# Kernel optimization log

Measured on AMD Instinct MI355X. Metric: run time of the kernel, lower is better.

The kernel has to match this reference:

```python
import jax, jax.numpy as jnp
import numpy as np

N, E = 100000, 800000
H, C = 4, 32
HC = H * C


def setup_inputs() -> dict:
    key = jax.random.key(0)
    ks = jax.random.split(key, 32)

    def lin(k, fi, fo):
        return jax.random.normal(k, (fi, fo), jnp.float32) / np.sqrt(fi)

    inp = {
        "x": jax.random.normal(ks[0], (N, 2), jnp.float32),
        "edge_index": jax.random.randint(ks[1], (2, E), 0, N, jnp.int64),
        "edge_attr": jax.random.normal(ks[2], (E, 1), jnp.float32),
        # layer 0 (in=2)
        "Wq0": lin(ks[3], 2, HC), "bq0": jnp.zeros((HC,), jnp.float32),
        "Wk0": lin(ks[4], 2, HC), "bk0": jnp.zeros((HC,), jnp.float32),
        "Wv0": lin(ks[5], 2, HC), "bv0": jnp.zeros((HC,), jnp.float32),
        "We0": lin(ks[6], 1, HC),
        "Ws0": lin(ks[7], 2, HC), "bs0": jnp.zeros((HC,), jnp.float32),
        # layer 1 (in=HC)
        "Wq1": lin(ks[8], HC, HC), "bq1": jnp.zeros((HC,), jnp.float32),
        "Wk1": lin(ks[9], HC, HC), "bk1": jnp.zeros((HC,), jnp.float32),
        "Wv1": lin(ks[10], HC, HC), "bv1": jnp.zeros((HC,), jnp.float32),
        "We1": lin(ks[11], 1, HC),
        "Ws1": lin(ks[12], HC, HC), "bs1": jnp.zeros((HC,), jnp.float32),
        # classifier
        "Wc1": lin(ks[13], HC, 128), "bc1": jnp.zeros((128,), jnp.float32),
        "Wc2": lin(ks[14], 128, 64), "bc2": jnp.zeros((64,), jnp.float32),
        "Wc3": lin(ks[15], 64, 1), "bc3": jnp.zeros((1,), jnp.float32),
    }
    return inp


def _tconv(x, src, dst, edge_attr, Wq, bq, Wk, bk, Wv, bv, We, Ws, bs):
    # PyG TransformerConv (concat=True, root_weight=True, beta=False)
    n = x.shape[0]
    q = (x @ Wq + bq).reshape(n, H, C)
    k = (x @ Wk + bk).reshape(n, H, C)
    v = (x @ Wv + bv).reshape(n, H, C)
    e = (edge_attr @ We).reshape(-1, H, C)            # [E,H,C]
    k_j = k[src] + e
    v_j = v[src] + e
    alpha = jnp.einsum("ehc,ehc->eh", q[dst], k_j) / np.sqrt(C)  # [E,H]
    m = jax.ops.segment_max(alpha, dst, num_segments=n)          # [n,H]
    m = jnp.where(jnp.isfinite(m), m, 0.0)            # nodes with no in-edges
    ex = jnp.exp(alpha - m[dst])
    denom = jax.ops.segment_sum(ex, dst, num_segments=n)
    w = ex / (denom[dst] + 1e-16)                      # per-edge softmax weight
    out = jax.ops.segment_sum(v_j * w[:, :, None], dst, num_segments=n)
    return out.reshape(n, HC) + x @ Ws + bs


def reference(x, edge_index, edge_attr,
              Wq0, bq0, Wk0, bk0, Wv0, bv0, We0, Ws0, bs0,
              Wq1, bq1, Wk1, bk1, Wv1, bv1, We1, Ws1, bs1,
              Wc1, bc1, Wc2, bc2, Wc3, bc3):
    src, dst = edge_index[0], edge_index[1]
    h = jax.nn.relu(_tconv(x, src, dst, edge_attr, Wq0, bq0, Wk0, bk0, Wv0, bv0, We0, Ws0, bs0))
    h = jax.nn.relu(_tconv(h, src, dst, edge_attr, Wq1, bq1, Wk1, bk1, Wv1, bv1, We1, Ws1, bs1))
    # classifier (dropout inactive in eval)
    h = jax.nn.relu(h @ Wc1 + bc1)
    h = jax.nn.relu(h @ Wc2 + bc2)
    return h @ Wc3 + bc3
```

## Files before the change

kernel.cpp:

```cpp
#include <hip/hip_runtime.h>
#include <hip/hip_bf16.h>
#include <cstdio>
#include <cstdint>


typedef short s16x8 __attribute__((ext_vector_type(8)));
typedef float f32x4 __attribute__((ext_vector_type(4)));

static inline int cdiv(int a, int b) { return (a + b - 1) / b; }

#define EXP2F(x) __builtin_amdgcn_exp2f(x)
#define LOG2E 1.4426950408889634f
#define RSC 0.17677669529663687f

__device__ __forceinline__ float bflo(unsigned u) {
    union { unsigned i; float f; } x; x.i = u << 16; return x.f;
}
__device__ __forceinline__ float bfhi(unsigned u) {
    union { unsigned i; float f; } x; x.i = u & 0xffff0000u; return x.f;
}
__device__ __forceinline__ unsigned short f2b(float f) {
    __hip_bfloat16 h = __float2bfloat16(f);
    return *reinterpret_cast<unsigned short*>(&h);
}
__device__ __forceinline__ unsigned packbf(float lo, float hi) {
    return (unsigned)f2b(lo) | ((unsigned)f2b(hi) << 16);
}


__global__ __launch_bounds__(256) void hist_kernel(const int* __restrict__ dst, int E,
                                                   int* __restrict__ counts) {
    int e = blockIdx.x * 256 + threadIdx.x;
    if (e < E) atomicAdd(&counts[dst[e]], 1);
}

__global__ __launch_bounds__(256) void scan_sums(const int* __restrict__ counts, int n,
                                                 int* __restrict__ bsums) {
    __shared__ int red[256];
    int base = blockIdx.x * 2048 + threadIdx.x * 8;
    int s = 0;
#pragma unroll
    for (int j = 0; j < 8; ++j) {
        int i = base + j;
        if (i < n) s += counts[i];
    }
    red[threadIdx.x] = s;
    __syncthreads();
    for (int off = 128; off > 0; off >>= 1) {
        if (threadIdx.x < off) red[threadIdx.x] += red[threadIdx.x + off];
        __syncthreads();
    }
    if (threadIdx.x == 0) bsums[blockIdx.x] = red[0];
}

__global__ void scan_mid(int* bsums, int nb, int* offsets, int n) {
    if (blockIdx.x == 0 && threadIdx.x == 0) {
        int run = 0;
        for (int i = 0; i < nb; ++i) { int t = bsums[i]; bsums[i] = run; run += t; }
        offsets[n] = run;
    }
}

__global__ __launch_bounds__(256) void scan_out(const int* __restrict__ counts, int n,
                                                const int* __restrict__ bsums,
                                                int* __restrict__ offsets) {
    __shared__ int tsum[256];
    int base = blockIdx.x * 2048 + threadIdx.x * 8;
    int v[8];
    int s = 0;
#pragma unroll
    for (int j = 0; j < 8; ++j) {
        int i = base + j;
        v[j] = (i < n) ? counts[i] : 0;
        s += v[j];
    }
    tsum[threadIdx.x] = s;
    __syncthreads();
    for (int off = 1; off < 256; off <<= 1) {
        int x = (threadIdx.x >= (unsigned)off) ? tsum[threadIdx.x - off] : 0;
        __syncthreads();
        tsum[threadIdx.x] += x;
        __syncthreads();
    }
    int excl = tsum[threadIdx.x] - s + bsums[blockIdx.x];
#pragma unroll
    for (int j = 0; j < 8; ++j) {
        int i = base + j;
        if (i < n) { offsets[i] = excl; excl += v[j]; }
    }
}

__global__ __launch_bounds__(256) void scatter_kernel(const int* __restrict__ src,
                                                      const int* __restrict__ dst,
                                                      const float* __restrict__ ea, int E,
                                                      const int* __restrict__ offsets,
                                                      int* __restrict__ counts,
                                                      int* __restrict__ csr_off,
                                                      float* __restrict__ csr_ea) {
    int e = blockIdx.x * 256 + threadIdx.x;
    if (e >= E) return;
    int d = dst[e];
    int r = atomicSub(&counts[d], 1);
    int p = offsets[d] + r - 1;
    csr_off[p] = src[e] << 9;
    csr_ea[p] = ea[e];
}


__global__ __launch_bounds__(256) void pack_w_kernel(
    const float* __restrict__ Wq1, const float* __restrict__ Wk1,
    const float* __restrict__ Wv1, const float* __restrict__ Ws1,
    const float* __restrict__ Wc1, const float* __restrict__ Wc2,
    unsigned short* __restrict__ wpk,
    const float* __restrict__ Wq0, const float* __restrict__ bq0,
    const float* __restrict__ Wk0, const float* __restrict__ bk0,
    const float* __restrict__ We0, float* __restrict__ gcoef) {
    if (blockIdx.x == 352) {
        int t = threadIdx.x;
        if (t < 48) {
            int h = t / 12, r = t % 12, i = r >> 2, j = r & 3;
            const float* A = (i == 0) ? Wq0 : (i == 1) ? (Wq0 + 128) : bq0;
            const float* B = (j == 0) ? Wk0 : (j == 1) ? (Wk0 + 128) : (j == 2) ? We0 : bk0;
            float s = 0.f;
            for (int c = 0; c < 32; ++c) s += A[h * 32 + c] * B[h * 32 + c];
            gcoef[h * 12 + i * 4 + j] = s * (RSC * LOG2E);
        }
        return;
    }
    int idx = blockIdx.x * 256 + threadIdx.x;
    int local, COLS;
    const float* W;
    if (idx < 81920) {
        int m = idx >> 14;
        local = idx & 16383;
        COLS = 128;
        W = (m == 0) ? Wq1 : (m == 1) ? Wk1 : (m == 2) ? Wv1 : (m == 3) ? Ws1 : Wc1;
    } else {
        local = idx - 81920;
        COLS = 64;
        W = Wc2;
    }
    int CT = COLS >> 4;
    int j = local & 7, lane = (local >> 3) & 63, t = local >> 9;
    int ct = t % CT, kc = t / CT;
    int k = kc * 32 + ((lane >> 4) << 3) + j;
    int nn = (ct << 4) + (lane & 15);
    wpk[idx] = f2b(W[k * COLS + nn]);
}


__global__ __launch_bounds__(256) void agg0_kernel(
    const float* __restrict__ x, const float* __restrict__ gcoef,
    float4* __restrict__ agg4,
    const int* __restrict__ offsets, const int* __restrict__ csr_off,
    const float* __restrict__ csr_ea, int n_nodes) {
    int tid = blockIdx.x * 256 + threadIdx.x;
    int n = tid >> 2, h = tid & 3;
    if (n >= n_nodes) return;
    float2 xn = ((const float2*)x)[n];
    const float4* G4 = (const float4*)gcoef;
    float4 g0 = G4[h * 3 + 0], g1 = G4[h * 3 + 1], g2 = G4[h * 3 + 2];
    float c0 = fmaf(xn.y, g1.x, fmaf(xn.x, g0.x, g2.x));
    float c1 = fmaf(xn.y, g1.y, fmaf(xn.x, g0.y, g2.y));
    float c2 = fmaf(xn.y, g1.z, fmaf(xn.x, g0.z, g2.z));
    float c3 = fmaf(xn.y, g1.w, fmaf(xn.x, g0.w, g2.w));
    int beg = offsets[n], end = offsets[n + 1];
    float d = 0.f, X0 = 0.f, X1 = 0.f, EA = 0.f;
    for (int j = beg; j < end; ++j) {
        int off = csr_off[j];
        float e = csr_ea[j];
        float2 xs = *(const float2*)((const char*)x + (off >> 6));
        float al = fmaf(c0, xs.x, fmaf(c1, xs.y, fmaf(c2, e, c3)));
        float w = EXP2F(fminf(al, 72.f));
        d += w;
        X0 = fmaf(w, xs.x, X0);
        X1 = fmaf(w, xs.y, X1);
        EA = fmaf(w, e, EA);
    }
    agg4[(size_t)n * 4 + h] = make_float4(X0, X1, EA, d);
}


__global__ __launch_bounds__(256) void expand0_kernel(
    const float* __restrict__ x, const float4* __restrict__ agg4,
    const float* __restrict__ Wv, const float* __restrict__ bv,
    const float* __restrict__ We, const float* __restrict__ Ws,
    const float* __restrict__ bs, uint2* __restrict__ H0, int n_nodes) {
    int gid = blockIdx.x * 256 + threadIdx.x;
    int n = gid >> 5, g = gid & 31;
    if (n >= n_nodes) return;
    int h = g >> 3;
    float4 ag = agg4[(size_t)n * 4 + h];
    float inv = 1.f / (ag.w + 1e-16f);
    float2 xn = ((const float2*)x)[n];
    float4 wv0 = ((const float4*)Wv)[g], wv1 = ((const float4*)(Wv + 128))[g];
    float4 we = ((const float4*)We)[g], bv4 = ((const float4*)bv)[g];
    float4 ws0 = ((const float4*)Ws)[g], ws1 = ((const float4*)(Ws + 128))[g];
    float4 bs4 = ((const float4*)bs)[g];
    float o0 = fmaf(wv0.x, ag.x, fmaf(wv1.x, ag.y, fmaf(we.x, ag.z, bv4.x * ag.w))) * inv
             + fmaf(xn.x, ws0.x, fmaf(xn.y, ws1.x, bs4.x));
    float o1 = fmaf(wv0.y, ag.x, fmaf(wv1.y, ag.y, fmaf(we.y, ag.z, bv4.y * ag.w))) * inv
             + fmaf(xn.x, ws0.y, fmaf(xn.y, ws1.y, bs4.y));
    float o2 = fmaf(wv0.z, ag.x, fmaf(wv1.z, ag.y, fmaf(we.z, ag.z, bv4.z * ag.w))) * inv
             + fmaf(xn.x, ws0.z, fmaf(xn.y, ws1.z, bs4.z));
    float o3 = fmaf(wv0.w, ag.x, fmaf(wv1.w, ag.y, fmaf(we.w, ag.z, bv4.w * ag.w))) * inv
             + fmaf(xn.x, ws0.w, fmaf(xn.y, ws1.w, bs4.w));
    uint2 o;
    o.x = packbf(fmaxf(o0, 0.f), fmaxf(o1, 0.f));
    o.y = packbf(fmaxf(o2, 0.f), fmaxf(o3, 0.f));
    H0[(size_t)n * 32 + g] = o;
}


__global__ __launch_bounds__(64) void agg1_kernel(
    const uint2* __restrict__ Q2, const unsigned short* __restrict__ KV,
    const float* __restrict__ We, const uint2* __restrict__ S2,
    uint2* __restrict__ Hout, const int* __restrict__ offsets,
    const int* __restrict__ csr_off, const float* __restrict__ csr_ea,
    int n_nodes) {
    int lane = threadIdx.x & 63;
    int h = lane & 31, half = lane >> 5;
    int n = blockIdx.x;
    if (n >= n_nodes) return;
    size_t rb = (size_t)n * 32;
    const float sc = RSC * LOG2E;
    uint2 qp = Q2[rb + h];
    float q0 = bflo(qp.x) * sc, q1 = bfhi(qp.x) * sc;
    float q2 = bflo(qp.y) * sc, q3 = bfhi(qp.y) * sc;
    float4 we4 = ((const float4*)We)[h];
    float qwe = fmaf(q3, we4.w, fmaf(q2, we4.z, fmaf(q1, we4.y, q0 * we4.x)));
    qwe += __shfl_xor(qwe, 1);
    qwe += __shfl_xor(qwe, 2);
    qwe += __shfl_xor(qwe, 4);
    int beg = __builtin_amdgcn_readfirstlane(offsets[n]);
    int end = __builtin_amdgcn_readfirstlane(offsets[n + 1]);
    float dA = 0.f, a0A = 0.f, a1A = 0.f, a2A = 0.f, a3A = 0.f, eA = 0.f;
    float dB = 0.f, a0B = 0.f, a1B = 0.f, a2B = 0.f, a3B = 0.f, eB = 0.f;
    int lane_b = h << 3;
    for (int j = beg + half; j < end; j += 4) {
        int jB = j + 2;
        bool vB = jB < end;
        int jmB = vB ? jB : j;
        int offA = csr_off[j], offB = csr_off[jmB];
        float eaA = csr_ea[j], eaB = csr_ea[jmB];
        const char* kvA = (const char*)KV + (size_t)(unsigned)offA + lane_b;
        const char* kvB = (const char*)KV + (size_t)(unsigned)offB + lane_b;
        uint2 kA = *(const uint2*)kvA;
        uint2 vA = *(const uint2*)(kvA + 256);
        uint2 kB = *(const uint2*)kvB;
        uint2 vB2 = *(const uint2*)(kvB + 256);
        {
            float p = fmaf(q3, bfhi(kA.y), fmaf(q2, bflo(kA.y),
                      fmaf(q1, bfhi(kA.x), q0 * bflo(kA.x))));
            p += __shfl_xor(p, 1);
            p += __shfl_xor(p, 2);
            p += __shfl_xor(p, 4);
            float al = fminf(fmaf(eaA, qwe, p), 72.f);
            float w = EXP2F(al);
            dA += w;
            a0A = fmaf(w, bflo(vA.x), a0A);
            a1A = fmaf(w, bfhi(vA.x), a1A);
            a2A = fmaf(w, bflo(vA.y), a2A);
            a3A = fmaf(w, bfhi(vA.y), a3A);
            eA = fmaf(w, eaA, eA);
        }
        {
            float p = fmaf(q3, bfhi(kB.y), fmaf(q2, bflo(kB.y),
                      fmaf(q1, bfhi(kB.x), q0 * bflo(kB.x))));
            p += __shfl_xor(p, 1);
            p += __shfl_xor(p, 2);
            p += __shfl_xor(p, 4);
            float al = fmaf(eaB, qwe, p);
            al = vB ? al : -3.0e38f;
            float w = EXP2F(fminf(al, 72.f));
            dB += w;
            a0B = fmaf(w, bflo(vB2.x), a0B);
            a1B = fmaf(w, bfhi(vB2.x), a1B);
            a2B = fmaf(w, bflo(vB2.y), a2B);
            a3B = fmaf(w, bfhi(vB2.y), a3B);
            eB = fmaf(w, eaB, eB);
        }
    }
    float d = dA + dB;
    float a0 = a0A + a0B, a1 = a1A + a1B, a2 = a2A + a2B, a3 = a3A + a3B;
    float ea = eA + eB;
    d += __shfl_xor(d, 32);
    a0 += __shfl_xor(a0, 32);
    a1 += __shfl_xor(a1, 32);
    a2 += __shfl_xor(a2, 32);
    a3 += __shfl_xor(a3, 32);
    ea += __shfl_xor(ea, 32);
    if (half == 0) {
        float inv = 1.f / (d + 1e-16f);
        uint2 sp = S2[rb + h];
        uint2 o;
        o.x = packbf(fmaxf(fmaf(a0 + we4.x * ea, inv, bflo(sp.x)), 0.f),
                     fmaxf(fmaf(a1 + we4.y * ea, inv, bfhi(sp.x)), 0.f));
        o.y = packbf(fmaxf(fmaf(a2 + we4.z * ea, inv, bflo(sp.y)), 0.f),
                     fmaxf(fmaf(a3 + we4.w * ea, inv, bfhi(sp.y)), 0.f));
        Hout[rb + h] = o;
    }
}


__global__ __launch_bounds__(256, 2) void gemm4_kernel(
    const unsigned short* __restrict__ Hb, int n_nodes,
    const unsigned short* __restrict__ wpk,
    const float* __restrict__ B0, unsigned short* __restrict__ O0, int ld0,
    const float* __restrict__ B1, unsigned short* __restrict__ O1, int ld1,
    const float* __restrict__ B2, unsigned short* __restrict__ O2, int ld2,
    const float* __restrict__ B3, unsigned short* __restrict__ O3, int ld3) {
    __shared__ unsigned short wbuf[16384];
    __shared__ char tbuf[128 * 272];
    int tid = threadIdx.x;
    int wid = tid >> 6, lane = tid & 63;
    int lr = lane & 15, lk = lane >> 4;
    int nblk = blockIdx.x * 128;

    s16x8 b[2][4];
#pragma unroll
    for (int nt = 0; nt < 2; ++nt) {
        int row = min(nblk + wid * 32 + nt * 16 + lr, n_nodes - 1);
        const s16x8* hp = (const s16x8*)(Hb + (size_t)row * 128);
#pragma unroll
        for (int kc = 0; kc < 4; ++kc) b[nt][kc] = hp[kc * 4 + lk];
    }
    const float* Bm[4] = {B0, B1, B2, B3};
    unsigned short* Om[4] = {O0, O1, O2, O3};
    int ldm[4] = {ld0, ld1, ld2, ld3};

#pragma unroll
    for (int i = 0; i < 8; ++i) {
        int c = i * 256 + tid;
        ((uint4*)wbuf)[c] = ((const uint4*)wpk)[c];
    }
#pragma unroll
    for (int mm = 0; mm < 4; ++mm) {
        __syncthreads();
        f32x4 acc[2][8];
#pragma unroll
        for (int nt = 0; nt < 2; ++nt)
#pragma unroll
            for (int ct = 0; ct < 8; ++ct) acc[nt][ct] = (f32x4){0.f, 0.f, 0.f, 0.f};
#pragma unroll
        for (int kc = 0; kc < 4; ++kc) {
#pragma unroll
            for (int ct = 0; ct < 8; ++ct) {
                s16x8 a = ((const s16x8*)wbuf)[(kc * 8 + ct) * 64 + lane];
                acc[0][ct] = __builtin_amdgcn_mfma_f32_16x16x32_bf16(a, b[0][kc], acc[0][ct], 0, 0, 0);
                acc[1][ct] = __builtin_amdgcn_mfma_f32_16x16x32_bf16(a, b[1][kc], acc[1][ct], 0, 0, 0);
            }
        }
        const float* Bp = Bm[mm];
#pragma unroll
        for (int ct = 0; ct < 8; ++ct) {
            float4 bb = *(const float4*)(Bp + ct * 16 + lk * 4);
#pragma unroll
            for (int nt = 0; nt < 2; ++nt) {
                int rnode = wid * 32 + nt * 16 + lr;
                uint2 o;
                o.x = packbf(acc[nt][ct][0] + bb.x, acc[nt][ct][1] + bb.y);
                o.y = packbf(acc[nt][ct][2] + bb.z, acc[nt][ct][3] + bb.w);
                *(uint2*)(tbuf + rnode * 272 + ct * 32 + lk * 8) = o;
            }
        }
        __syncthreads();
        unsigned short* Op = Om[mm];
        int ld = ldm[mm];
#pragma unroll
        for (int i = 0; i < 8; ++i) {
            int chunk = i * 256 + tid;
            int nd = chunk >> 4, c16 = chunk & 15;
            int ng = nblk + nd;
            uint4 v = *(const uint4*)(tbuf + nd * 272 + c16 * 16);
            if (ng < n_nodes) *(uint4*)(Op + (size_t)ng * ld + c16 * 8) = v;
        }
        if (mm < 3) {
            const uint4* ws = (const uint4*)(wpk + (mm + 1) * 16384);
#pragma unroll
            for (int i = 0; i < 8; ++i) {
                int c = i * 256 + tid;
                ((uint4*)wbuf)[c] = ws[c];
            }
        }
    }
}


__global__ __launch_bounds__(256) void classifier_kernel(
    const unsigned short* __restrict__ H1b, int n_nodes,
    const unsigned short* __restrict__ wc1p, const float* __restrict__ bc1,
    const unsigned short* __restrict__ wc2p, const float* __restrict__ bc2,
    const float* __restrict__ Wc3, const float* __restrict__ bc3,
    float* __restrict__ out) {
    __shared__ char lds_raw[4 * 16 * 272];
    int wid = threadIdx.x >> 6, lane = threadIdx.x & 63;
    int lr = lane & 15, lk = lane >> 4;
    int nb = blockIdx.x * 64 + wid * 16;
    char* tile = lds_raw + wid * 16 * 272;

    s16x8 b[4];
    {
        int row = min(nb + lr, n_nodes - 1);
        const s16x8* hp = (const s16x8*)(H1b + (size_t)row * 128);
#pragma unroll
        for (int kc = 0; kc < 4; ++kc) b[kc] = hp[kc * 4 + lk];
    }
    f32x4 acc[8];
#pragma unroll
    for (int ct = 0; ct < 8; ++ct) acc[ct] = (f32x4){0.f, 0.f, 0.f, 0.f};
#pragma unroll
    for (int kc = 0; kc < 4; ++kc)
#pragma unroll
        for (int ct = 0; ct < 8; ++ct) {
            s16x8 a = ((const s16x8*)wc1p)[(kc * 8 + ct) * 64 + lane];
            acc[ct] = __builtin_amdgcn_mfma_f32_16x16x32_bf16(a, b[kc], acc[ct], 0, 0, 0);
        }
#pragma unroll
    for (int ct = 0; ct < 8; ++ct) {
        float4 bb = *(const float4*)(bc1 + ct * 16 + lk * 4);
        uint2 o;
        o.x = packbf(fmaxf(acc[ct][0] + bb.x, 0.f), fmaxf(acc[ct][1] + bb.y, 0.f));
        o.y = packbf(fmaxf(acc[ct][2] + bb.z, 0.f), fmaxf(acc[ct][3] + bb.w, 0.f));
        *(uint2*)(tile + lr * 272 + ct * 32 + lk * 8) = o;
    }
    __syncthreads();
    s16x8 b2[4];
#pragma unroll
    for (int kc = 0; kc < 4; ++kc)
        b2[kc] = *(const s16x8*)(tile + lr * 272 + kc * 64 + lk * 16);
    f32x4 acc2[4];
#pragma unroll
    for (int ct = 0; ct < 4; ++ct) acc2[ct] = (f32x4){0.f, 0.f, 0.f, 0.f};
#pragma unroll
    for (int kc = 0; kc < 4; ++kc)
#pragma unroll
        for (int ct = 0; ct < 4; ++ct) {
            s16x8 a = ((const s16x8*)wc2p)[(kc * 4 + ct) * 64 + lane];
            acc2[ct] = __builtin_amdgcn_mfma_f32_16x16x32_bf16(a, b2[kc], acc2[ct], 0, 0, 0);
        }
    float part = 0.f;
#pragma unroll
    for (int ct = 0; ct < 4; ++ct) {
        int ch0 = ct * 16 + lk * 4;
        float4 bb = *(const float4*)(bc2 + ch0);
        float4 w3 = *(const float4*)(Wc3 + ch0);
        part += fmaxf(acc2[ct][0] + bb.x, 0.f) * w3.x;
        part += fmaxf(acc2[ct][1] + bb.y, 0.f) * w3.y;
        part += fmaxf(acc2[ct][2] + bb.z, 0.f) * w3.z;
        part += fmaxf(acc2[ct][3] + bb.w, 0.f) * w3.w;
    }
    part += __shfl_xor(part, 16);
    part += __shfl_xor(part, 32);
    if (lk == 0) {
        int node = nb + lr;
        if (node < n_nodes) out[node] = part + bc3[0];
    }
}


extern "C" void kernel_launch(void* const* d_in, const int* in_sizes, int n_in,
                              void* d_out, int out_size, void* d_ws, size_t ws_size,
                              hipStream_t stream) {
    const float* x = (const float*)d_in[0];
    const int* ei = (const int*)d_in[1];
    const float* ea = (const float*)d_in[2];
    const float *Wq0 = (const float*)d_in[3], *bq0 = (const float*)d_in[4];
    const float *Wk0 = (const float*)d_in[5], *bk0 = (const float*)d_in[6];
    const float *Wv0 = (const float*)d_in[7], *bv0 = (const float*)d_in[8];
    const float* We0 = (const float*)d_in[9];
    const float *Ws0 = (const float*)d_in[10], *bs0 = (const float*)d_in[11];
    const float *Wq1 = (const float*)d_in[12], *bq1 = (const float*)d_in[13];
    const float *Wk1 = (const float*)d_in[14], *bk1 = (const float*)d_in[15];
    const float *Wv1 = (const float*)d_in[16], *bv1 = (const float*)d_in[17];
    const float* We1 = (const float*)d_in[18];
    const float *Ws1 = (const float*)d_in[19], *bs1 = (const float*)d_in[20];
    const float *Wc1 = (const float*)d_in[21], *bc1 = (const float*)d_in[22];
    const float *Wc2 = (const float*)d_in[23], *bc2 = (const float*)d_in[24];
    const float *Wc3 = (const float*)d_in[25], *bc3 = (const float*)d_in[26];

    const int N = in_sizes[0] / 2;
    const int E = in_sizes[2];
    const int* src = ei;
    const int* dst = ei + E;

    size_t NM = (size_t)N * 128;
    float4* agg4 = (float4*)d_ws;
    float* gcoef = (float*)(agg4 + (size_t)N * 4);
    unsigned short* H0b = (unsigned short*)(gcoef + 64);
    unsigned short* Qb = H0b + NM;
    unsigned short* KV = Qb + NM;
    unsigned short* S1b = KV + 2 * NM;
    unsigned short* wpk = S1b + NM;
    int* counts = (int*)(wpk + 90112);
    int* offsets = counts + N;
    int* bsums = offsets + N + 1;
    int* csr_off = bsums + 256;
    float* csr_ea = (float*)(csr_off + E);
    size_t need = (size_t)((char*)(csr_ea + E) - (char*)d_ws);
    if (need > ws_size) {
        fprintf(stderr, "kernel_launch: ws too small (need %zu, have %zu)\n", need, ws_size);
        return;
    }

    const int NB_SCAN = cdiv(N, 2048);

    hipMemsetAsync(counts, 0, (size_t)N * 4, stream);
    hist_kernel<<<cdiv(E, 256), 256, 0, stream>>>(dst, E, counts);
    scan_sums<<<NB_SCAN, 256, 0, stream>>>(counts, N, bsums);
    scan_mid<<<1, 64, 0, stream>>>(bsums, NB_SCAN, offsets, N);
    scan_out<<<NB_SCAN, 256, 0, stream>>>(counts, N, bsums, offsets);
    scatter_kernel<<<cdiv(E, 256), 256, 0, stream>>>(src, dst, ea, E, offsets, counts,
                                                     csr_off, csr_ea);
    pack_w_kernel<<<353, 256, 0, stream>>>(Wq1, Wk1, Wv1, Ws1, Wc1, Wc2, wpk,
                                           Wq0, bq0, Wk0, bk0, We0, gcoef);

    agg0_kernel<<<cdiv(N * 4, 256), 256, 0, stream>>>(
        x, gcoef, agg4, offsets, csr_off, csr_ea, N);
    expand0_kernel<<<cdiv(N * 32, 256), 256, 0, stream>>>(
        x, agg4, Wv0, bv0, We0, Ws0, bs0, (uint2*)H0b, N);

    gemm4_kernel<<<cdiv(N, 128), 256, 0, stream>>>(
        H0b, N, wpk,
        bq1, Qb, 128,
        bk1, KV, 256,
        bv1, KV + 128, 256,
        bs1, S1b, 128);
    agg1_kernel<<<N, 64, 0, stream>>>(
        (const uint2*)Qb, KV, We1, (const uint2*)S1b, (uint2*)S1b,
        offsets, csr_off, csr_ea, N);

    classifier_kernel<<<cdiv(N, 64), 256, 0, stream>>>(
        S1b, N, wpk + 65536, bc1, wpk + 81920, bc2, Wc3, bc3, (float*)d_out);
}
```

Before: 353.1 us.

## Fuse preprocessing and layer-0 kernels, interleave CSR, stage classifier weights in LDS

The edge histogram is merged into the weight-packing kernel. The three-kernel prefix scan becomes one 1024-thread single-block scan, and the separate source-offset and edge-attribute CSR arrays are interleaved into one int2 array. The layer-0 aggregation and expansion kernels are fused through shared memory, which removes the agg4 intermediate buffer. agg1 now handles four nodes per 256-thread block, and the classifier copies its packed weights into LDS with a launch-bounds occupancy hint. The aim is fewer launches and less global traffic, at the cost of a serial single-block scan that depends on N fitting in 1024×100 entries.

```diff
diff --git a/kernel.cpp b/kernel.cpp
--- a/kernel.cpp
+++ b/kernel.cpp
@@ -28,86 +28,8 @@
 }
 
 
-__global__ __launch_bounds__(256) void hist_kernel(const int* __restrict__ dst, int E,
-                                                   int* __restrict__ counts) {
-    int e = blockIdx.x * 256 + threadIdx.x;
-    if (e < E) atomicAdd(&counts[dst[e]], 1);
-}
-
-__global__ __launch_bounds__(256) void scan_sums(const int* __restrict__ counts, int n,
-                                                 int* __restrict__ bsums) {
-    __shared__ int red[256];
-    int base = blockIdx.x * 2048 + threadIdx.x * 8;
-    int s = 0;
-#pragma unroll
-    for (int j = 0; j < 8; ++j) {
-        int i = base + j;
-        if (i < n) s += counts[i];
-    }
-    red[threadIdx.x] = s;
-    __syncthreads();
-    for (int off = 128; off > 0; off >>= 1) {
-        if (threadIdx.x < off) red[threadIdx.x] += red[threadIdx.x + off];
-        __syncthreads();
-    }
-    if (threadIdx.x == 0) bsums[blockIdx.x] = red[0];
-}
-
-__global__ void scan_mid(int* bsums, int nb, int* offsets, int n) {
-    if (blockIdx.x == 0 && threadIdx.x == 0) {
-        int run = 0;
-        for (int i = 0; i < nb; ++i) { int t = bsums[i]; bsums[i] = run; run += t; }
-        offsets[n] = run;
-    }
-}
-
-__global__ __launch_bounds__(256) void scan_out(const int* __restrict__ counts, int n,
-                                                const int* __restrict__ bsums,
-                                                int* __restrict__ offsets) {
-    __shared__ int tsum[256];
-    int base = blockIdx.x * 2048 + threadIdx.x * 8;
-    int v[8];
-    int s = 0;
-#pragma unroll
-    for (int j = 0; j < 8; ++j) {
-        int i = base + j;
-        v[j] = (i < n) ? counts[i] : 0;
-        s += v[j];
-    }
-    tsum[threadIdx.x] = s;
-    __syncthreads();
-    for (int off = 1; off < 256; off <<= 1) {
-        int x = (threadIdx.x >= (unsigned)off) ? tsum[threadIdx.x - off] : 0;
-        __syncthreads();
-        tsum[threadIdx.x] += x;
-        __syncthreads();
-    }
-    int excl = tsum[threadIdx.x] - s + bsums[blockIdx.x];
-#pragma unroll
-    for (int j = 0; j < 8; ++j) {
-        int i = base + j;
-        if (i < n) { offsets[i] = excl; excl += v[j]; }
-    }
-}
-
-__global__ __launch_bounds__(256) void scatter_kernel(const int* __restrict__ src,
-                                                      const int* __restrict__ dst,
-                                                      const float* __restrict__ ea, int E,
-                                                      const int* __restrict__ offsets,
-                                                      int* __restrict__ counts,
-                                                      int* __restrict__ csr_off,
-                                                      float* __restrict__ csr_ea) {
-    int e = blockIdx.x * 256 + threadIdx.x;
-    if (e >= E) return;
-    int d = dst[e];
-    int r = atomicSub(&counts[d], 1);
-    int p = offsets[d] + r - 1;
-    csr_off[p] = src[e] << 9;
-    csr_ea[p] = ea[e];
-}
-
-
-__global__ __launch_bounds__(256) void pack_w_kernel(
+__global__ __launch_bounds__(256) void histpack_kernel(
+    const int* __restrict__ dst, int E, int* __restrict__ counts, int nb_hist,
     const float* __restrict__ Wq1, const float* __restrict__ Wk1,
     const float* __restrict__ Wv1, const float* __restrict__ Ws1,
     const float* __restrict__ Wc1, const float* __restrict__ Wc2,
@@ -115,7 +37,14 @@
     const float* __restrict__ Wq0, const float* __restrict__ bq0,
     const float* __restrict__ Wk0, const float* __restrict__ bk0,
     const float* __restrict__ We0, float* __restrict__ gcoef) {
-    if (blockIdx.x == 352) {
+    int bid = blockIdx.x;
+    if (bid < nb_hist) {
+        int e = bid * 256 + threadIdx.x;
+        if (e < E) atomicAdd(&counts[dst[e]], 1);
+        return;
+    }
+    int pb = bid - nb_hist;
+    if (pb == 352) {
         int t = threadIdx.x;
         if (t < 48) {
             int h = t / 12, r = t % 12, i = r >> 2, j = r & 3;
@@ -127,7 +56,7 @@
         }
         return;
     }
-    int idx = blockIdx.x * 256 + threadIdx.x;
+    int idx = pb * 256 + threadIdx.x;
     int local, COLS;
     const float* W;
     if (idx < 81920) {
@@ -149,78 +78,126 @@
 }
 
 
-__global__ __launch_bounds__(256) void agg0_kernel(
+__global__ __launch_bounds__(1024) void scan1_kernel(const int* __restrict__ counts,
+                                                     int n, int* __restrict__ offsets) {
+    __shared__ int ts[1024];
+    const int CH = 100;
+    int t = threadIdx.x;
+    int base = t * CH;
+    int endi = min(base + CH, n);
+    int s = 0;
+    int i = base;
+    for (; i + 3 < endi; i += 4) {
+        int4 v = *(const int4*)(counts + i);
+        s += v.x + v.y + v.z + v.w;
+    }
+    for (; i < endi; ++i) s += counts[i];
+    ts[t] = s;
+    __syncthreads();
+    for (int off = 1; off < 1024; off <<= 1) {
+        int x = (t >= off) ? ts[t - off] : 0;
+        __syncthreads();
+        ts[t] += x;
+        __syncthreads();
+    }
+    if (t == 1023) offsets[n] = ts[1023];
+    int excl = ts[t] - s;
+    for (int k = base; k < endi; ++k) {
+        int c = counts[k];
+        offsets[k] = excl;
+        excl += c;
+    }
+}
+
+__global__ __launch_bounds__(256) void scatter_kernel(const int* __restrict__ src,
+                                                      const int* __restrict__ dst,
+                                                      const float* __restrict__ ea, int E,
+                                                      const int* __restrict__ offsets,
+                                                      int* __restrict__ counts,
+                                                      int2* __restrict__ csr) {
+    int e = blockIdx.x * 256 + threadIdx.x;
+    if (e >= E) return;
+    int d = dst[e];
+    int r = atomicSub(&counts[d], 1);
+    int p = offsets[d] + r - 1;
+    csr[p] = make_int2(src[e] << 9, __float_as_int(ea[e]));
+}
+
+
+__global__ __launch_bounds__(256) void agg0x_kernel(
     const float* __restrict__ x, const float* __restrict__ gcoef,
-    float4* __restrict__ agg4,
-    const int* __restrict__ offsets, const int* __restrict__ csr_off,
-    const float* __restrict__ csr_ea, int n_nodes) {
-    int tid = blockIdx.x * 256 + threadIdx.x;
-    int n = tid >> 2, h = tid & 3;
-    if (n >= n_nodes) return;
-    float2 xn = ((const float2*)x)[n];
-    const float4* G4 = (const float4*)gcoef;
-    float4 g0 = G4[h * 3 + 0], g1 = G4[h * 3 + 1], g2 = G4[h * 3 + 2];
-    float c0 = fmaf(xn.y, g1.x, fmaf(xn.x, g0.x, g2.x));
-    float c1 = fmaf(xn.y, g1.y, fmaf(xn.x, g0.y, g2.y));
-    float c2 = fmaf(xn.y, g1.z, fmaf(xn.x, g0.z, g2.z));
-    float c3 = fmaf(xn.y, g1.w, fmaf(xn.x, g0.w, g2.w));
-    int beg = offsets[n], end = offsets[n + 1];
-    float d = 0.f, X0 = 0.f, X1 = 0.f, EA = 0.f;
-    for (int j = beg; j < end; ++j) {
-        int off = csr_off[j];
-        float e = csr_ea[j];
-        float2 xs = *(const float2*)((const char*)x + (off >> 6));
-        float al = fmaf(c0, xs.x, fmaf(c1, xs.y, fmaf(c2, e, c3)));
-        float w = EXP2F(fminf(al, 72.f));
-        d += w;
-        X0 = fmaf(w, xs.x, X0);
-        X1 = fmaf(w, xs.y, X1);
-        EA = fmaf(w, e, EA);
-    }
-    agg4[(size_t)n * 4 + h] = make_float4(X0, X1, EA, d);
-}
-
-
-__global__ __launch_bounds__(256) void expand0_kernel(
-    const float* __restrict__ x, const float4* __restrict__ agg4,
     const float* __restrict__ Wv, const float* __restrict__ bv,
     const float* __restrict__ We, const float* __restrict__ Ws,
-    const float* __restrict__ bs, uint2* __restrict__ H0, int n_nodes) {
-    int gid = blockIdx.x * 256 + threadIdx.x;
-    int n = gid >> 5, g = gid & 31;
-    if (n >= n_nodes) return;
-    int h = g >> 3;
-    float4 ag = agg4[(size_t)n * 4 + h];
-    float inv = 1.f / (ag.w + 1e-16f);
-    float2 xn = ((const float2*)x)[n];
+    const float* __restrict__ bs, uint2* __restrict__ H0,
+    const int* __restrict__ offsets, const int2* __restrict__ csr, int n_nodes) {
+    __shared__ float4 sm[256];
+    int t = threadIdx.x;
+    int nb = blockIdx.x * 64;
+    {
+        int n = nb + (t >> 2), h = t & 3;
+        if (n < n_nodes) {
+            float2 xn = ((const float2*)x)[n];
+            const float4* G4 = (const float4*)gcoef;
+            float4 g0 = G4[h * 3 + 0], g1 = G4[h * 3 + 1], g2 = G4[h * 3 + 2];
+            float c0 = fmaf(xn.y, g1.x, fmaf(xn.x, g0.x, g2.x));
+            float c1 = fmaf(xn.y, g1.y, fmaf(xn.x, g0.y, g2.y));
+            float c2 = fmaf(xn.y, g1.z, fmaf(xn.x, g0.z, g2.z));
+            float c3 = fmaf(xn.y, g1.w, fmaf(xn.x, g0.w, g2.w));
+            int beg = offsets[n], end = offsets[n + 1];
+            float d = 0.f, X0 = 0.f, X1 = 0.f, EA = 0.f;
+            for (int j = beg; j < end; ++j) {
+                int2 ce = csr[j];
+                float e = __int_as_float(ce.y);
+                float2 xs = *(const float2*)((const char*)x + (((unsigned)ce.x) >> 6));
+                float al = fmaf(c0, xs.x, fmaf(c1, xs.y, fmaf(c2, e, c3)));
+                float w = EXP2F(fminf(al, 72.f));
+                d += w;
+                X0 = fmaf(w, xs.x, X0);
+                X1 = fmaf(w, xs.y, X1);
+                EA = fmaf(w, e, EA);
+            }
+            sm[t] = make_float4(X0, X1, EA, d);
+        }
+    }
+    __syncthreads();
+    int g = t & 31;
     float4 wv0 = ((const float4*)Wv)[g], wv1 = ((const float4*)(Wv + 128))[g];
     float4 we = ((const float4*)We)[g], bv4 = ((const float4*)bv)[g];
     float4 ws0 = ((const float4*)Ws)[g], ws1 = ((const float4*)(Ws + 128))[g];
     float4 bs4 = ((const float4*)bs)[g];
-    float o0 = fmaf(wv0.x, ag.x, fmaf(wv1.x, ag.y, fmaf(we.x, ag.z, bv4.x * ag.w))) * inv
-             + fmaf(xn.x, ws0.x, fmaf(xn.y, ws1.x, bs4.x));
-    float o1 = fmaf(wv0.y, ag.x, fmaf(wv1.y, ag.y, fmaf(we.y, ag.z, bv4.y * ag.w))) * inv
-             + fmaf(xn.x, ws0.y, fmaf(xn.y, ws1.y, bs4.y));
-    float o2 = fmaf(wv0.z, ag.x, fmaf(wv1.z, ag.y, fmaf(we.z, ag.z, bv4.z * ag.w))) * inv
-             + fmaf(xn.x, ws0.z, fmaf(xn.y, ws1.z, bs4.z));
-    float o3 = fmaf(wv0.w, ag.x, fmaf(wv1.w, ag.y, fmaf(we.w, ag.z, bv4.w * ag.w))) * inv
-             + fmaf(xn.x, ws0.w, fmaf(xn.y, ws1.w, bs4.w));
-    uint2 o;
-    o.x = packbf(fmaxf(o0, 0.f), fmaxf(o1, 0.f));
-    o.y = packbf(fmaxf(o2, 0.f), fmaxf(o3, 0.f));
-    H0[(size_t)n * 32 + g] = o;
-}
-
-
-__global__ __launch_bounds__(64) void agg1_kernel(
+    int h = g >> 3;
+#pragma unroll
+    for (int it = 0; it < 8; ++it) {
+        int ln = it * 8 + (t >> 5);
+        int n2 = nb + ln;
+        if (n2 >= n_nodes) break;
+        float4 ag = sm[ln * 4 + h];
+        float inv = 1.f / (ag.w + 1e-16f);
+        float2 xn = ((const float2*)x)[n2];
+        float o0 = fmaf(wv0.x, ag.x, fmaf(wv1.x, ag.y, fmaf(we.x, ag.z, bv4.x * ag.w))) * inv
+                 + fmaf(xn.x, ws0.x, fmaf(xn.y, ws1.x, bs4.x));
+        float o1 = fmaf(wv0.y, ag.x, fmaf(wv1.y, ag.y, fmaf(we.y, ag.z, bv4.y * ag.w))) * inv
+                 + fmaf(xn.x, ws0.y, fmaf(xn.y, ws1.y, bs4.y));
+        float o2 = fmaf(wv0.z, ag.x, fmaf(wv1.z, ag.y, fmaf(we.z, ag.z, bv4.z * ag.w))) * inv
+                 + fmaf(xn.x, ws0.z, fmaf(xn.y, ws1.z, bs4.z));
+        float o3 = fmaf(wv0.w, ag.x, fmaf(wv1.w, ag.y, fmaf(we.w, ag.z, bv4.w * ag.w))) * inv
+                 + fmaf(xn.x, ws0.w, fmaf(xn.y, ws1.w, bs4.w));
+        uint2 o;
+        o.x = packbf(fmaxf(o0, 0.f), fmaxf(o1, 0.f));
+        o.y = packbf(fmaxf(o2, 0.f), fmaxf(o3, 0.f));
+        H0[(size_t)n2 * 32 + g] = o;
+    }
+}
+
+
+__global__ __launch_bounds__(256) void agg1_kernel(
     const uint2* __restrict__ Q2, const unsigned short* __restrict__ KV,
     const float* __restrict__ We, const uint2* __restrict__ S2,
     uint2* __restrict__ Hout, const int* __restrict__ offsets,
-    const int* __restrict__ csr_off, const float* __restrict__ csr_ea,
-    int n_nodes) {
-    int lane = threadIdx.x & 63;
+    const int2* __restrict__ csr, int n_nodes) {
+    int wid = threadIdx.x >> 6, lane = threadIdx.x & 63;
     int h = lane & 31, half = lane >> 5;
-    int n = blockIdx.x;
+    int n = blockIdx.x * 4 + wid;
     if (n >= n_nodes) return;
     size_t rb = (size_t)n * 32;
     const float sc = RSC * LOG2E;
@@ -240,13 +217,13 @@
     for (int j = beg + half; j < end; j += 4) {
         int jB = j + 2;
         bool vB = jB < end;
-        int jmB = vB ? jB : j;
-        int offA = csr_off[j], offB = csr_off[jmB];
-        float eaA = csr_ea[j], eaB = csr_ea[jmB];
-        const char* kvA = (const char*)KV + (size_t)(unsigned)offA + lane_b;
-        const char* kvB = (const char*)KV + (size_t)(unsigned)offB + lane_b;
+        int2 ceA = csr[j];
+        int2 ceB = csr[vB ? jB : beg];
+        float eaA = __int_as_float(ceA.y), eaB = __int_as_float(ceB.y);
+        const char* kvA = (const char*)KV + (size_t)(unsigned)ceA.x + lane_b;
+        const char* kvB = (const char*)KV + (size_t)(unsigned)ceB.x + lane_b;
         uint2 kA = *(const uint2*)kvA;
-        uint2 vA = *(const uint2*)(kvA + 256);
+        uint2 vA2 = *(const uint2*)(kvA + 256);
         uint2 kB = *(const uint2*)kvB;
         uint2 vB2 = *(const uint2*)(kvB + 256);
         {
@@ -258,11 +235,11 @@
             float al = fminf(fmaf(eaA, qwe, p), 72.f);
             float w = EXP2F(al);
             dA += w;
-            a0A = fmaf(w, bflo(vA.x), a0A);
-            a1A = fmaf(w, bfhi(vA.x), a1A);
-            a2A = fmaf(w, bflo(vA.y), a2A);
-            a3A = fmaf(w, bfhi(vA.y), a3A);
             eA = fmaf(w, eaA, eA);
+            a0A = fmaf(w, bflo(vA2.x), a0A);
+            a1A = fmaf(w, bfhi(vA2.x), a1A);
+            a2A = fmaf(w, bflo(vA2.y), a2A);
+            a3A = fmaf(w, bfhi(vA2.y), a3A);
         }
         {
             float p = fmaf(q3, bfhi(kB.y), fmaf(q2, bflo(kB.y),
@@ -274,30 +251,29 @@
             al = vB ? al : -3.0e38f;
             float w = EXP2F(fminf(al, 72.f));
             dB += w;
+            eB = fmaf(w, eaB, eB);
             a0B = fmaf(w, bflo(vB2.x), a0B);
             a1B = fmaf(w, bfhi(vB2.x), a1B);
             a2B = fmaf(w, bflo(vB2.y), a2B);
             a3B = fmaf(w, bfhi(vB2.y), a3B);
-            eB = fmaf(w, eaB, eB);
-        }
-    }
-    float d = dA + dB;
+        }
+    }
+    float d = dA + dB, ea = eA + eB;
     float a0 = a0A + a0B, a1 = a1A + a1B, a2 = a2A + a2B, a3 = a3A + a3B;
-    float ea = eA + eB;
     d += __shfl_xor(d, 32);
+    ea += __shfl_xor(ea, 32);
     a0 += __shfl_xor(a0, 32);
     a1 += __shfl_xor(a1, 32);
     a2 += __shfl_xor(a2, 32);
     a3 += __shfl_xor(a3, 32);
-    ea += __shfl_xor(ea, 32);
     if (half == 0) {
         float inv = 1.f / (d + 1e-16f);
         uint2 sp = S2[rb + h];
         uint2 o;
-        o.x = packbf(fmaxf(fmaf(a0 + we4.x * ea, inv, bflo(sp.x)), 0.f),
-                     fmaxf(fmaf(a1 + we4.y * ea, inv, bfhi(sp.x)), 0.f));
-        o.y = packbf(fmaxf(fmaf(a2 + we4.z * ea, inv, bflo(sp.y)), 0.f),
-                     fmaxf(fmaf(a3 + we4.w * ea, inv, bfhi(sp.y)), 0.f));
+        o.x = packbf(fmaxf(fmaf(fmaf(we4.x, ea, a0), inv, bflo(sp.x)), 0.f),
+                     fmaxf(fmaf(fmaf(we4.y, ea, a1), inv, bfhi(sp.x)), 0.f));
+        o.y = packbf(fmaxf(fmaf(fmaf(we4.z, ea, a2), inv, bflo(sp.y)), 0.f),
+                     fmaxf(fmaf(fmaf(we4.w, ea, a3), inv, bfhi(sp.y)), 0.f));
         Hout[rb + h] = o;
     }
 }
@@ -310,8 +286,8 @@
     const float* __restrict__ B1, unsigned short* __restrict__ O1, int ld1,
     const float* __restrict__ B2, unsigned short* __restrict__ O2, int ld2,
     const float* __restrict__ B3, unsigned short* __restrict__ O3, int ld3) {
-    __shared__ unsigned short wbuf[16384];
-    __shared__ char tbuf[128 * 272];
+    __shared__ __align__(16) unsigned short wbuf[16384];
+    __shared__ __align__(16) char tbuf[128 * 272];
     int tid = threadIdx.x;
     int wid = tid >> 6, lane = tid & 63;
     int lr = lane & 15, lk = lane >> 4;
@@ -387,17 +363,27 @@
 }
 
 
-__global__ __launch_bounds__(256) void classifier_kernel(
+__global__ __launch_bounds__(256, 2) void classifier_kernel(
     const unsigned short* __restrict__ H1b, int n_nodes,
     const unsigned short* __restrict__ wc1p, const float* __restrict__ bc1,
     const unsigned short* __restrict__ wc2p, const float* __restrict__ bc2,
     const float* __restrict__ Wc3, const float* __restrict__ bc3,
     float* __restrict__ out) {
-    __shared__ char lds_raw[4 * 16 * 272];
-    int wid = threadIdx.x >> 6, lane = threadIdx.x & 63;
+    __shared__ __align__(16) unsigned short w1s[16384];
+    __shared__ __align__(16) unsigned short w2s[8192];
+    __shared__ __align__(16) char lds_raw[4 * 16 * 272];
+    int tid = threadIdx.x;
+    int wid = tid >> 6, lane = tid & 63;
     int lr = lane & 15, lk = lane >> 4;
     int nb = blockIdx.x * 64 + wid * 16;
     char* tile = lds_raw + wid * 16 * 272;
+
+#pragma unroll
+    for (int i = 0; i < 8; ++i)
+        ((uint4*)w1s)[i * 256 + tid] = ((const uint4*)wc1p)[i * 256 + tid];
+#pragma unroll
+    for (int i = 0; i < 4; ++i)
+        ((uint4*)w2s)[i * 256 + tid] = ((const uint4*)wc2p)[i * 256 + tid];
 
     s16x8 b[4];
     {
@@ -406,6 +392,7 @@
 #pragma unroll
         for (int kc = 0; kc < 4; ++kc) b[kc] = hp[kc * 4 + lk];
     }
+    __syncthreads();
     f32x4 acc[8];
 #pragma unroll
     for (int ct = 0; ct < 8; ++ct) acc[ct] = (f32x4){0.f, 0.f, 0.f, 0.f};
@@ -413,7 +400,7 @@
     for (int kc = 0; kc < 4; ++kc)
 #pragma unroll
         for (int ct = 0; ct < 8; ++ct) {
-            s16x8 a = ((const s16x8*)wc1p)[(kc * 8 + ct) * 64 + lane];
+            s16x8 a = ((const s16x8*)w1s)[(kc * 8 + ct) * 64 + lane];
             acc[ct] = __builtin_amdgcn_mfma_f32_16x16x32_bf16(a, b[kc], acc[ct], 0, 0, 0);
         }
 #pragma unroll
@@ -436,7 +423,7 @@
     for (int kc = 0; kc < 4; ++kc)
 #pragma unroll
         for (int ct = 0; ct < 4; ++ct) {
-            s16x8 a = ((const s16x8*)wc2p)[(kc * 4 + ct) * 64 + lane];
+            s16x8 a = ((const s16x8*)w2s)[(kc * 4 + ct) * 64 + lane];
             acc2[ct] = __builtin_amdgcn_mfma_f32_16x16x32_bf16(a, b2[kc], acc2[ct], 0, 0, 0);
         }
     float part = 0.f;
@@ -485,8 +472,7 @@
     const int* dst = ei + E;
 
     size_t NM = (size_t)N * 128;
-    float4* agg4 = (float4*)d_ws;
-    float* gcoef = (float*)(agg4 + (size_t)N * 4);
+    float* gcoef = (float*)d_ws;
     unsigned short* H0b = (unsigned short*)(gcoef + 64);
     unsigned short* Qb = H0b + NM;
     unsigned short* KV = Qb + NM;
@@ -494,31 +480,24 @@
     unsigned short* wpk = S1b + NM;
     int* counts = (int*)(wpk + 90112);
     int* offsets = counts + N;
-    int* bsums = offsets + N + 1;
-    int* csr_off = bsums + 256;
-    float* csr_ea = (float*)(csr_off + E);
-    size_t need = (size_t)((char*)(csr_ea + E) - (char*)d_ws);
+    int2* csr = (int2*)(offsets + N + 2);
+    size_t need = (size_t)((char*)(csr + E) - (char*)d_ws);
     if (need > ws_size) {
         fprintf(stderr, "kernel_launch: ws too small (need %zu, have %zu)\n", need, ws_size);
         return;
     }
 
-    const int NB_SCAN = cdiv(N, 2048);
+    const int NB_HIST = cdiv(E, 256);
 
     hipMemsetAsync(counts, 0, (size_t)N * 4, stream);
-    hist_kernel<<<cdiv(E, 256), 256, 0, stream>>>(dst, E, counts);
-    scan_sums<<<NB_SCAN, 256, 0, stream>>>(counts, N, bsums);
-    scan_mid<<<1, 64, 0, stream>>>(bsums, NB_SCAN, offsets, N);
-    scan_out<<<NB_SCAN, 256, 0, stream>>>(counts, N, bsums, offsets);
-    scatter_kernel<<<cdiv(E, 256), 256, 0, stream>>>(src, dst, ea, E, offsets, counts,
-                                                     csr_off, csr_ea);
-    pack_w_kernel<<<353, 256, 0, stream>>>(Wq1, Wk1, Wv1, Ws1, Wc1, Wc2, wpk,
-                                           Wq0, bq0, Wk0, bk0, We0, gcoef);
-
-    agg0_kernel<<<cdiv(N * 4, 256), 256, 0, stream>>>(
-        x, gcoef, agg4, offsets, csr_off, csr_ea, N);
-    expand0_kernel<<<cdiv(N * 32, 256), 256, 0, stream>>>(
-        x, agg4, Wv0, bv0, We0, Ws0, bs0, (uint2*)H0b, N);
+    histpack_kernel<<<NB_HIST + 353, 256, 0, stream>>>(
+        dst, E, counts, NB_HIST, Wq1, Wk1, Wv1, Ws1, Wc1, Wc2, wpk,
+        Wq0, bq0, Wk0, bk0, We0, gcoef);
+    scan1_kernel<<<1, 1024, 0, stream>>>(counts, N, offsets);
+    scatter_kernel<<<NB_HIST, 256, 0, stream>>>(src, dst, ea, E, offsets, counts, csr);
+
+    agg0x_kernel<<<cdiv(N, 64), 256, 0, stream>>>(
+        x, gcoef, Wv0, bv0, We0, Ws0, bs0, (uint2*)H0b, offsets, csr, N);
 
     gemm4_kernel<<<cdiv(N, 128), 256, 0, stream>>>(
         H0b, N, wpk,
@@ -526,9 +505,9 @@
         bk1, KV, 256,
         bv1, KV + 128, 256,
         bs1, S1b, 128);
-    agg1_kernel<<<N, 64, 0, stream>>>(
+    agg1_kernel<<<cdiv(N, 4), 256, 0, stream>>>(
         (const uint2*)Qb, KV, We1, (const uint2*)S1b, (uint2*)S1b,
-        offsets, csr_off, csr_ea, N);
+        offsets, csr, N);
 
     classifier_kernel<<<cdiv(N, 64), 256, 0, stream>>>(
         S1b, N, wpk + 65536, bc1, wpk + 81920, bc2, Wc3, bc3, (float*)d_out);
```

Result: slower. 462.9 us (+31.1%).
